# Kernel tuning notes

Hardware: AMD Instinct MI355X
Metric: run time of the kernel (lower is better)

The kernel has to match this reference:

```python
import jax, jax.numpy as jnp
import numpy as np

SUB1 = 0.5
SUB2 = 0.2

def setup_inputs() -> dict:
    key = jax.random.key(0)
    kx, kw, kb = jax.random.split(key, 3)
    x = jax.random.normal(kx, (32, 16, 256, 256), dtype=jnp.float32)
    # Conv2d weight [C_out, C_in, K, K], PyTorch default init scale ~ 1/sqrt(fan_in)
    fan_in = 16 * 3 * 3
    bound = 1.0 / np.sqrt(fan_in)
    conv_weight = jax.random.uniform(kw, (16, 16, 3, 3), dtype=jnp.float32, minval=-bound, maxval=bound)
    conv_bias = jax.random.uniform(kb, (16,), dtype=jnp.float32, minval=-bound, maxval=bound)
    return {"x": x, "conv_weight": conv_weight, "conv_bias": conv_bias}

def mish(v):
    # mish(v) = v * tanh(softplus(v))
    return v * jnp.tanh(jax.nn.softplus(v))

def reference(x, conv_weight, conv_bias):
    # valid conv, stride 1, NCHW / OIHW
    y = jax.lax.conv_general_dilated(
        x, conv_weight,
        window_strides=(1, 1),
        padding='VALID',
        dimension_numbers=('NCHW', 'OIHW', 'NCHW'))
    y = y + conv_bias[None, :, None, None]
    y = y - (SUB1 + SUB2)
    return mish(y)
```

## Files before the change

### kernel.cpp

```cpp
#include <hip/hip_runtime.h>
#include <hip/hip_bf16.h>

constexpr int N  = 32;
constexpr int C  = 16;
constexpr int H  = 256;
constexpr int W  = 256;
constexpr int CO = 16;
constexpr int KS = 3;
constexpr int OH = 254;
constexpr int OW = 254;

constexpr float SUBV = 0.7f;

constexpr int TW = 64;
constexpr int TH = 16;
constexpr int CICHUNK = 4;
constexpr int IN_W = TW + 4;
constexpr int IN_H = TH + 2;
constexpr int QUADS_PER_ROW = IN_W / 4;
constexpr int STAGE_QUADS = CICHUNK * IN_H * QUADS_PER_ROW;

__global__ void reorder_weights(const float* __restrict__ w,
                                const float* __restrict__ b,
                                float* __restrict__ wr) {
    const int t = threadIdx.x;
    for (int i = t; i < C * KS * KS * CO; i += blockDim.x) {
        const int co   = i % CO;
        const int rest = i / CO;
        const int kx   = rest % 3;
        const int ky   = (rest / 3) % 3;
        const int ci   = rest / 9;
        wr[i] = w[((co * C + ci) * KS + ky) * KS + kx];
    }
    if (t < CO) wr[C * KS * KS * CO + t] = b[t] - SUBV;
}

__launch_bounds__(256, 4)
__global__ void conv_mish(const float* __restrict__ x,
                          const float* __restrict__ wr,
                          float* __restrict__ out) {
    __shared__ float lds[CICHUNK * IN_H * IN_W];

    const int tid = threadIdx.x;
    const int x0  = blockIdx.x * TW;
    const int oy0 = blockIdx.y * TH;
    const int n   = blockIdx.z;

    const int col = tid & 15;
    const int py  = tid >> 4;
    const int px0 = col * 4;

    float acc[4][CO];
#pragma unroll
    for (int p = 0; p < 4; ++p)
#pragma unroll
        for (int co = 0; co < CO; ++co) acc[p][co] = 0.0f;

    for (int cc = 0; cc < C; cc += CICHUNK) {
        if (cc) __syncthreads();

        const float* src = x + ((size_t)(n * C + cc) * H) * W;
        for (int q = tid; q < STAGE_QUADS; q += 256) {
            const int ciq  = q / (IN_H * QUADS_PER_ROW);
            int rem        = q - ciq * (IN_H * QUADS_PER_ROW);
            const int row  = rem / QUADS_PER_ROW;
            const int quad = rem - row * QUADS_PER_ROW;
            int iy = oy0 + row;      if (iy > H - 1) iy = H - 1;
            int ix = x0 + quad * 4;  if (ix > W - 4) ix = W - 4;
            const float4 v = *(const float4*)(src + ((size_t)ciq * H + iy) * W + ix);
            *(float4*)(&lds[(ciq * IN_H + row) * IN_W + quad * 4]) = v;
        }
        __syncthreads();

#pragma unroll
        for (int ci = 0; ci < CICHUNK; ++ci) {
            float in[3][6];
#pragma unroll
            for (int r = 0; r < 3; ++r) {
                const float* p = &lds[(ci * IN_H + py + r) * IN_W + px0];
                const float4 a = *(const float4*)p;
                const float2 bl = *(const float2*)(p + 4);
                in[r][0] = a.x; in[r][1] = a.y; in[r][2] = a.z; in[r][3] = a.w;
                in[r][4] = bl.x; in[r][5] = bl.y;
            }
            const float* wp = wr + (cc + ci) * 9 * CO;
#pragma unroll
            for (int ky = 0; ky < 3; ++ky) {
#pragma unroll
                for (int kx = 0; kx < 3; ++kx) {
#pragma unroll
                    for (int co = 0; co < CO; ++co) {
                        const float wv = wp[(ky * 3 + kx) * CO + co];
#pragma unroll
                        for (int p = 0; p < 4; ++p)
                            acc[p][co] = fmaf(in[ky][kx + p], wv, acc[p][co]);
                    }
                }
            }
        }
    }

    const int oy = oy0 + py;
    if (oy < OH) {
#pragma unroll
        for (int co = 0; co < CO; ++co) {
            const float bias = wr[C * KS * KS * CO + co];
            float* orow = out + ((size_t)(n * CO + co) * OH + oy) * OW;
#pragma unroll
            for (int p = 0; p < 4; ++p) {
                const int ox = x0 + px0 + p;
                if (ox < OW) {
                    const float v  = acc[p][co] + bias;
                    const float vc = fminf(v, 15.0f);
                    const float e  = __expf(vc);
                    const float z  = 1.0f + e;
                    const float z2 = z * z;
                    const float t  = __fdividef(z2 - 1.0f, z2 + 1.0f);
                    orow[ox] = v * t;
                }
            }
        }
    }
}

extern "C" void kernel_launch(void* const* d_in, const int* in_sizes, int n_in,
                              void* d_out, int out_size, void* d_ws, size_t ws_size,
                              hipStream_t stream) {
    const float* x = (const float*)d_in[0];
    const float* w = (const float*)d_in[1];
    const float* b = (const float*)d_in[2];
    float* out = (float*)d_out;
    float* wr  = (float*)d_ws;

    hipLaunchKernelGGL(reorder_weights, dim3(1), dim3(256), 0, stream, w, b, wr);

    dim3 grid((OW + TW - 1) / TW, (OH + TH - 1) / TH, N);
    hipLaunchKernelGGL(conv_mish, grid, dim3(256), 0, stream, x, wr, out);
}
```

Before: 351.8 us.

## Split output channels across two thread halves and vectorize output stores

Doubles the block to 512 threads, with each half computing 8 of the 16 output channels for the same spatial tile. This halves the per-thread accumulators to lower register pressure and raise occupancy, at the cost of duplicated LDS input reads. The per-half channel index goes through readfirstlane so weight loads stay scalar. Output writes become float4 stores where the row allows. Because the output row stride is 254 floats, those float4 stores can be misaligned.

```diff
diff --git a/kernel.cpp b/kernel.cpp
--- a/kernel.cpp
+++ b/kernel.cpp
@@ -20,6 +20,8 @@
 constexpr int QUADS_PER_ROW = IN_W / 4;
 constexpr int STAGE_QUADS = CICHUNK * IN_H * QUADS_PER_ROW;
 
+constexpr int BLK = 512;
+
 __global__ void reorder_weights(const float* __restrict__ w,
                                 const float* __restrict__ b,
                                 float* __restrict__ wr) {
@@ -35,7 +37,7 @@
     if (t < CO) wr[C * KS * KS * CO + t] = b[t] - SUBV;
 }
 
-__launch_bounds__(256, 4)
+__launch_bounds__(BLK, 4)
 __global__ void conv_mish(const float* __restrict__ x,
                           const float* __restrict__ wr,
                           float* __restrict__ out) {
@@ -47,20 +49,22 @@
     const int n   = blockIdx.z;
 
     const int col = tid & 15;
-    const int py  = tid >> 4;
+    const int py  = (tid >> 4) & 15;
+    const int coh = __builtin_amdgcn_readfirstlane(tid >> 8);
     const int px0 = col * 4;
 
-    float acc[4][CO];
+    float acc[4][8];
 #pragma unroll
     for (int p = 0; p < 4; ++p)
 #pragma unroll
-        for (int co = 0; co < CO; ++co) acc[p][co] = 0.0f;
+        for (int co = 0; co < 8; ++co) acc[p][co] = 0.0f;
 
+#pragma unroll 1
     for (int cc = 0; cc < C; cc += CICHUNK) {
         if (cc) __syncthreads();
 
         const float* src = x + ((size_t)(n * C + cc) * H) * W;
-        for (int q = tid; q < STAGE_QUADS; q += 256) {
+        for (int q = tid; q < STAGE_QUADS; q += BLK) {
             const int ciq  = q / (IN_H * QUADS_PER_ROW);
             int rem        = q - ciq * (IN_H * QUADS_PER_ROW);
             const int row  = rem / QUADS_PER_ROW;
@@ -78,18 +82,18 @@
 #pragma unroll
             for (int r = 0; r < 3; ++r) {
                 const float* p = &lds[(ci * IN_H + py + r) * IN_W + px0];
-                const float4 a = *(const float4*)p;
+                const float4 a  = *(const float4*)p;
                 const float2 bl = *(const float2*)(p + 4);
                 in[r][0] = a.x; in[r][1] = a.y; in[r][2] = a.z; in[r][3] = a.w;
                 in[r][4] = bl.x; in[r][5] = bl.y;
             }
-            const float* wp = wr + (cc + ci) * 9 * CO;
+            const float* wp = wr + (cc + ci) * 9 * CO + coh * 8;
 #pragma unroll
             for (int ky = 0; ky < 3; ++ky) {
 #pragma unroll
                 for (int kx = 0; kx < 3; ++kx) {
 #pragma unroll
-                    for (int co = 0; co < CO; ++co) {
+                    for (int co = 0; co < 8; ++co) {
                         const float wv = wp[(ky * 3 + kx) * CO + co];
 #pragma unroll
                         for (int p = 0; p < 4; ++p)
@@ -102,22 +106,28 @@
 
     const int oy = oy0 + py;
     if (oy < OH) {
+        const int ox = x0 + px0;
 #pragma unroll
-        for (int co = 0; co < CO; ++co) {
-            const float bias = wr[C * KS * KS * CO + co];
-            float* orow = out + ((size_t)(n * CO + co) * OH + oy) * OW;
+        for (int co = 0; co < 8; ++co) {
+            const int gco = coh * 8 + co;
+            const float bias = wr[C * KS * KS * CO + gco];
+            float* orow = out + ((size_t)(n * CO + gco) * OH + oy) * OW;
+            float r[4];
 #pragma unroll
             for (int p = 0; p < 4; ++p) {
-                const int ox = x0 + px0 + p;
-                if (ox < OW) {
-                    const float v  = acc[p][co] + bias;
-                    const float vc = fminf(v, 15.0f);
-                    const float e  = __expf(vc);
-                    const float z  = 1.0f + e;
-                    const float z2 = z * z;
-                    const float t  = __fdividef(z2 - 1.0f, z2 + 1.0f);
-                    orow[ox] = v * t;
-                }
+                const float v  = acc[p][co] + bias;
+                const float vc = fminf(v, 15.0f);
+                const float e  = __expf(vc);
+                const float z  = 1.0f + e;
+                const float z2 = z * z;
+                r[p] = v * __fdividef(z2 - 1.0f, z2 + 1.0f);
+            }
+            if (ox + 3 < OW) {
+                *(float4*)(orow + ox) = make_float4(r[0], r[1], r[2], r[3]);
+            } else {
+#pragma unroll
+                for (int p = 0; p < 4; ++p)
+                    if (ox + p < OW) orow[ox + p] = r[p];
             }
         }
     }
@@ -135,5 +145,5 @@
     hipLaunchKernelGGL(reorder_weights, dim3(1), dim3(256), 0, stream, w, b, wr);
 
     dim3 grid((OW + TW - 1) / TW, (OH + TH - 1) / TH, N);
-    hipLaunchKernelGGL(conv_mish, grid, dim3(256), 0, stream, x, wr, out);
+    hipLaunchKernelGGL(conv_mish, grid, dim3(BLK), 0, stream, x, wr, out);
 }
```

Measured after the change: 337.3 us. 1.04x faster.
